# Kernel tuning notes

Measured on AMD Instinct MI355X. Metric: run time of the kernel, lower is better.

The kernel has to match this reference:

```python
import jax, jax.numpy as jnp
import numpy as np

B, N, D = 32, 32768, 128

def setup_inputs() -> dict:
    key = jax.random.key(0)
    k1, k2, k3 = jax.random.split(key, 3)
    inputs = jax.random.normal(k1, (B, D), dtype=jnp.float32)
    # alphas must be in (0,1): variance = 1 - alpha
    alphas = jax.random.uniform(k2, (B,), dtype=jnp.float32, minval=0.05, maxval=0.95)
    data_batch = jax.random.normal(k3, (N, D), dtype=jnp.float32)
    return {"inputs": inputs, "alphas": alphas, "data_batch": data_batch}

def reference(inputs, alphas, data_batch):
    # inputs: [B, D], alphas: [B], data_batch: [N, D]
    d = inputs.shape[-1]
    sqrt_a = jnp.sqrt(alphas)[:, None]          # [B, 1]
    var = (1.0 - alphas)[:, None]                # [B, 1]
    # means = sqrt(alpha) * data -> [B, N, D]; squared distance summed over D
    diff = inputs[:, None, :] - sqrt_a[:, :, None] * data_batch[None]  # [B, N, D]
    sq = jnp.sum(diff * diff, axis=-1)           # [B, N]
    # logits summed over feature dim: -(0.5*D*log(var) + 0.5/var * sq)
    logits = -(0.5 * d * jnp.log(var) + 0.5 / var * sq)  # [B, N]
    probs = jax.nn.softmax(logits, axis=1)       # [B, N]
    x0 = probs @ data_batch                      # [B, D]
    return (inputs - sqrt_a * x0) / jnp.sqrt(var)
```

## Files before the change

kernel.cpp:

```cpp
#include <hip/hip_runtime.h>
#include <math.h>

#define BB 32
#define DD 128
#define NN 32768

#define NB1 1024
#define T1 256
#define ROWS 32
#define WS_STRIDE 132
#define NP NB1

__global__ __launch_bounds__(T1) void bayes_k1(
    const float* __restrict__ inputs, const float* __restrict__ alphas,
    const float* __restrict__ data, float* __restrict__ ws)
{
    __shared__ float4 tile[ROWS * 32];
    __shared__ float  ms[2][16][2];

    const int tid  = threadIdx.x;
    const int lane = tid & 63;
    const int wv   = tid >> 6;
    const int half = wv >> 1;
    const int wr   = wv & 1;
    const int br   = lane >> 2;
    const int q    = lane & 3;
    const int b    = half * 16 + br;
    const int bid  = blockIdx.x;

    const float alpha = alphas[b];
    const float sa    = sqrtf(alpha);
    const float var   = 1.0f - alpha;
    const float c1    = sa / var;
    const float c2    = 0.5f * alpha / var;

    const float4* g4 = (const float4*)data + (size_t)bid * (ROWS * DD / 4);
    {
        float4 v[4];
        #pragma unroll
        for (int k = 0; k < 4; ++k) v[k] = g4[k * T1 + tid];
        #pragma unroll
        for (int k = 0; k < 4; ++k) {
            const int f = k * T1 + tid;
            const int r = f >> 5, c = f & 31;
            tile[r * 32 + (c ^ ((r & 7) << 2))] = v[k];
        }
    }

    float4 in4[8];
    {
        const float4* ig = (const float4*)inputs + b * 32;
        #pragma unroll
        for (int j = 0; j < 8; ++j) in4[j] = ig[4 * j + q];
    }

    __syncthreads();

    float nn = 0.0f;
    {
        const int r = wr * 16 + (lane >> 2);
        const int sw = (r & 7) << 2;
        #pragma unroll
        for (int j = 0; j < 8; ++j) {
            const float4 d = tile[r * 32 + ((4 * j + q) ^ sw)];
            nn = fmaf(d.x, d.x, nn); nn = fmaf(d.y, d.y, nn);
            nn = fmaf(d.z, d.z, nn); nn = fmaf(d.w, d.w, nn);
        }
        nn += __shfl_xor(nn, 1);
        nn += __shfl_xor(nn, 2);
    }

    float m = -INFINITY, s = 0.0f;
    float4 acc[8];
    #pragma unroll
    for (int j = 0; j < 8; ++j) acc[j] = make_float4(0.f, 0.f, 0.f, 0.f);

    #pragma unroll 4
    for (int rl = 0; rl < 16; ++rl) {
        const int r  = wr * 16 + rl;
        const int sw = (r & 7) << 2;

        float4 d4[8];
        #pragma unroll
        for (int j = 0; j < 8; ++j) d4[j] = tile[r * 32 + ((4 * j + q) ^ sw)];

        float4 dv = make_float4(0.f, 0.f, 0.f, 0.f);
        #pragma unroll
        for (int j = 0; j < 8; ++j) {
            dv.x = fmaf(in4[j].x, d4[j].x, dv.x);
            dv.y = fmaf(in4[j].y, d4[j].y, dv.y);
            dv.z = fmaf(in4[j].z, d4[j].z, dv.z);
            dv.w = fmaf(in4[j].w, d4[j].w, dv.w);
        }
        float dot = (dv.x + dv.y) + (dv.z + dv.w);
        dot += __shfl_xor(dot, 1);
        dot += __shfl_xor(dot, 2);

        const float nr    = __shfl(nn, rl << 2);
        const float logit = c1 * dot - c2 * nr;

        float pp = logit - m;
        if (pp > 10.0f) {
            const float sc = __expf(-pp);
            s *= sc;
            #pragma unroll
            for (int j = 0; j < 8; ++j) {
                acc[j].x *= sc; acc[j].y *= sc; acc[j].z *= sc; acc[j].w *= sc;
            }
            m = logit; pp = 0.0f;
        }
        const float wgt = __expf(pp);
        s += wgt;
        #pragma unroll
        for (int j = 0; j < 8; ++j) {
            acc[j].x = fmaf(wgt, d4[j].x, acc[j].x);
            acc[j].y = fmaf(wgt, d4[j].y, acc[j].y);
            acc[j].z = fmaf(wgt, d4[j].z, acc[j].z);
            acc[j].w = fmaf(wgt, d4[j].w, acc[j].w);
        }
    }

    __syncthreads();
    float* red = (float*)tile;
    if (wr == 1) {
        if (q == 0) { ms[half][br][0] = m; ms[half][br][1] = s; }
        float4* rp = (float4*)(red + half * 2048 + br * 128);
        const int sw = (br & 7) << 2;
        #pragma unroll
        for (int j = 0; j < 8; ++j) rp[(4 * j + q) ^ sw] = acc[j];
    }
    __syncthreads();
    if (wr == 0) {
        const float mo = ms[half][br][0], so = ms[half][br][1];
        const float M  = fmaxf(m, mo);
        const float e0 = __expf(m - M), e1 = __expf(mo - M);
        s = s * e0 + so * e1;
        const float4* rp = (const float4*)(red + half * 2048 + br * 128);
        const int sw = (br & 7) << 2;
        #pragma unroll
        for (int j = 0; j < 8; ++j) {
            const float4 d = rp[(4 * j + q) ^ sw];
            acc[j].x = acc[j].x * e0 + e1 * d.x;
            acc[j].y = acc[j].y * e0 + e1 * d.y;
            acc[j].z = acc[j].z * e0 + e1 * d.z;
            acc[j].w = acc[j].w * e0 + e1 * d.w;
        }
        m = M;

        float* wsp = ws + ((size_t)bid * BB + b) * WS_STRIDE;
        if (q == 0) { wsp[0] = m; wsp[1] = s; }
        float4* wa = (float4*)(wsp + 4);
        #pragma unroll
        for (int j = 0; j < 8; ++j) wa[4 * j + q] = acc[j];
    }
}

__global__ __launch_bounds__(256) void bayes_k2(
    const float* __restrict__ inputs, const float* __restrict__ alphas,
    const float* __restrict__ ws, float* __restrict__ out)
{
    const int b   = blockIdx.x >> 2;
    const int dq  = blockIdx.x & 3;
    const int tid = threadIdx.x;

    __shared__ float e_s[NP];
    __shared__ float red_s[16];
    __shared__ float part[8][32];

    float mi[4], si[4];
    #pragma unroll
    for (int k = 0; k < 4; ++k) {
        const int i = tid + k * 256;
        const size_t idx = ((size_t)i * BB + b) * WS_STRIDE;
        mi[k] = ws[idx];
        si[k] = ws[idx + 1];
    }

    float mm = fmaxf(fmaxf(mi[0], mi[1]), fmaxf(mi[2], mi[3]));
    #pragma unroll
    for (int off = 1; off <= 32; off <<= 1) mm = fmaxf(mm, __shfl_xor(mm, off));
    if ((tid & 63) == 0) red_s[tid >> 6] = mm;
    __syncthreads();
    const float M = fmaxf(fmaxf(red_s[0], red_s[1]), fmaxf(red_s[2], red_s[3]));

    float ss = 0.0f;
    #pragma unroll
    for (int k = 0; k < 4; ++k) {
        const float ei = __expf(mi[k] - M);
        e_s[tid + k * 256] = ei;
        ss = fmaf(si[k], ei, ss);
    }
    #pragma unroll
    for (int off = 1; off <= 32; off <<= 1) ss += __shfl_xor(ss, off);
    if ((tid & 63) == 0) red_s[8 + (tid >> 6)] = ss;
    __syncthreads();
    const float S = (red_s[8] + red_s[9]) + (red_s[10] + red_s[11]);

    const int dd = tid & 31, ii = tid >> 5;
    const int d  = dq * 32 + dd;
    float x = 0.0f;
    #pragma unroll 8
    for (int k = 0; k < 128; ++k) {
        const int i = ii + k * 8;
        x = fmaf(e_s[i], ws[((size_t)i * BB + b) * WS_STRIDE + 4 + d], x);
    }
    part[ii][dd] = x;
    __syncthreads();

    if (tid < 32) {
        float x0 = 0.0f;
        #pragma unroll
        for (int p = 0; p < 8; ++p) x0 += part[p][tid];
        x0 /= S;
        const float alpha = alphas[b];
        const float sa  = sqrtf(alpha);
        const float var = 1.0f - alpha;
        const int dout  = dq * 32 + tid;
        out[b * DD + dout] = (inputs[b * DD + dout] - sa * x0) / sqrtf(var);
    }
}

extern "C" void kernel_launch(void* const* d_in, const int* in_sizes, int n_in,
                              void* d_out, int out_size, void* d_ws, size_t ws_size,
                              hipStream_t stream)
{
    const float* inputs = (const float*)d_in[0];
    const float* alphas = (const float*)d_in[1];
    const float* data   = (const float*)d_in[2];
    float* out = (float*)d_out;
    float* ws  = (float*)d_ws;

    bayes_k1<<<NB1, T1, 0, stream>>>(inputs, alphas, data, ws);
    bayes_k2<<<BB * 4, 256, 0, stream>>>(inputs, alphas, ws, out);
}
```

Baseline: 97.17 us.

## Compute logits and weighted sums with bf16 MFMA using split-precision operands

Rewrites the partial-softmax kernel so the data-input dot products run on MFMA 16x16x32 bf16 instructions. Both data and inputs are split into hi and lo bf16 parts to keep close to fp32 accuracy, and the probability-weighted sum runs as a second MFMA using bf16 exps and transposed data. Each block now covers 64 rows with one-shot softmax instead of 32 rows with online rescaling, which halves the partial count that the combine kernel reads, and the workspace layout becomes batch-major. The cost is bf16 rounding in the second GEMM, a strided transposed global load, and a much larger LDS footprint that can lower occupancy.

```diff
diff --git a/kernel.cpp b/kernel.cpp
--- a/kernel.cpp
+++ b/kernel.cpp
@@ -5,153 +5,249 @@
 #define DD 128
 #define NN 32768
 
-#define NB1 1024
-#define T1 256
-#define ROWS 32
-#define WS_STRIDE 132
-#define NP NB1
-
-__global__ __launch_bounds__(T1) void bayes_k1(
+#define NB 512
+#define RPB 64
+#define WS_STRIDE 136
+#define NP NB
+
+typedef __attribute__((ext_vector_type(8))) short bf16x8;
+typedef __attribute__((ext_vector_type(4))) float f32x4;
+
+#define O_RH   0
+#define O_RL   16384
+#define O_INH  32768
+#define O_INL  40960
+#define O_RT   49152
+#define O_D1   65536
+#define O_NRM  75776
+#define O_PT   O_INH
+#define O_X0   O_RH
+#define ARENA  76032
+
+__device__ __forceinline__ unsigned bf16_rne(float x) {
+    unsigned u = __builtin_bit_cast(unsigned, x);
+    return (u + 0x7FFFu + ((u >> 16) & 1u)) >> 16;
+}
+__device__ __forceinline__ float bf16f(unsigned h) {
+    return __builtin_bit_cast(float, h << 16);
+}
+__device__ __forceinline__ unsigned pk2(float a, float b) {
+    return bf16_rne(a) | (bf16_rne(b) << 16);
+}
+
+__global__ __launch_bounds__(256) void bayes_k1(
     const float* __restrict__ inputs, const float* __restrict__ alphas,
     const float* __restrict__ data, float* __restrict__ ws)
 {
-    __shared__ float4 tile[ROWS * 32];
-    __shared__ float  ms[2][16][2];
+    __shared__ __align__(16) char arena[ARENA];
 
     const int tid  = threadIdx.x;
     const int lane = tid & 63;
     const int wv   = tid >> 6;
-    const int half = wv >> 1;
-    const int wr   = wv & 1;
-    const int br   = lane >> 2;
-    const int q    = lane & 3;
-    const int b    = half * 16 + br;
+    const int ln   = lane & 15;
+    const int g    = lane >> 4;
     const int bid  = blockIdx.x;
 
-    const float alpha = alphas[b];
-    const float sa    = sqrtf(alpha);
-    const float var   = 1.0f - alpha;
-    const float c1    = sa / var;
-    const float c2    = 0.5f * alpha / var;
-
-    const float4* g4 = (const float4*)data + (size_t)bid * (ROWS * DD / 4);
-    {
-        float4 v[4];
-        #pragma unroll
-        for (int k = 0; k < 4; ++k) v[k] = g4[k * T1 + tid];
-        #pragma unroll
-        for (int k = 0; k < 4; ++k) {
-            const int f = k * T1 + tid;
-            const int r = f >> 5, c = f & 31;
-            tile[r * 32 + (c ^ ((r & 7) << 2))] = v[k];
-        }
-    }
-
-    float4 in4[8];
-    {
-        const float4* ig = (const float4*)inputs + b * 32;
-        #pragma unroll
-        for (int j = 0; j < 8; ++j) in4[j] = ig[4 * j + q];
-    }
-
-    __syncthreads();
-
-    float nn = 0.0f;
-    {
-        const int r = wr * 16 + (lane >> 2);
-        const int sw = (r & 7) << 2;
-        #pragma unroll
-        for (int j = 0; j < 8; ++j) {
-            const float4 d = tile[r * 32 + ((4 * j + q) ^ sw)];
-            nn = fmaf(d.x, d.x, nn); nn = fmaf(d.y, d.y, nn);
-            nn = fmaf(d.z, d.z, nn); nn = fmaf(d.w, d.w, nn);
-        }
+    {
+        const int r = tid >> 2, c4 = tid & 3;
+        const float4* gp = (const float4*)(data + ((size_t)bid * RPB + r) * DD + c4 * 32);
+        float v[32];
+        #pragma unroll
+        for (int i = 0; i < 8; ++i) {
+            const float4 t4 = gp[i];
+            v[4*i+0] = t4.x; v[4*i+1] = t4.y; v[4*i+2] = t4.z; v[4*i+3] = t4.w;
+        }
+        float nn = 0.0f;
+        #pragma unroll
+        for (int i = 0; i < 32; ++i) nn = fmaf(v[i], v[i], nn);
         nn += __shfl_xor(nn, 1);
         nn += __shfl_xor(nn, 2);
-    }
-
-    float m = -INFINITY, s = 0.0f;
-    float4 acc[8];
-    #pragma unroll
-    for (int j = 0; j < 8; ++j) acc[j] = make_float4(0.f, 0.f, 0.f, 0.f);
-
-    #pragma unroll 4
-    for (int rl = 0; rl < 16; ++rl) {
-        const int r  = wr * 16 + rl;
-        const int sw = (r & 7) << 2;
-
-        float4 d4[8];
-        #pragma unroll
-        for (int j = 0; j < 8; ++j) d4[j] = tile[r * 32 + ((4 * j + q) ^ sw)];
-
-        float4 dv = make_float4(0.f, 0.f, 0.f, 0.f);
-        #pragma unroll
-        for (int j = 0; j < 8; ++j) {
-            dv.x = fmaf(in4[j].x, d4[j].x, dv.x);
-            dv.y = fmaf(in4[j].y, d4[j].y, dv.y);
-            dv.z = fmaf(in4[j].z, d4[j].z, dv.z);
-            dv.w = fmaf(in4[j].w, d4[j].w, dv.w);
-        }
-        float dot = (dv.x + dv.y) + (dv.z + dv.w);
-        dot += __shfl_xor(dot, 1);
-        dot += __shfl_xor(dot, 2);
-
-        const float nr    = __shfl(nn, rl << 2);
-        const float logit = c1 * dot - c2 * nr;
-
-        float pp = logit - m;
-        if (pp > 10.0f) {
-            const float sc = __expf(-pp);
-            s *= sc;
-            #pragma unroll
-            for (int j = 0; j < 8; ++j) {
-                acc[j].x *= sc; acc[j].y *= sc; acc[j].z *= sc; acc[j].w *= sc;
-            }
-            m = logit; pp = 0.0f;
-        }
-        const float wgt = __expf(pp);
-        s += wgt;
-        #pragma unroll
-        for (int j = 0; j < 8; ++j) {
-            acc[j].x = fmaf(wgt, d4[j].x, acc[j].x);
-            acc[j].y = fmaf(wgt, d4[j].y, acc[j].y);
-            acc[j].z = fmaf(wgt, d4[j].z, acc[j].z);
-            acc[j].w = fmaf(wgt, d4[j].w, acc[j].w);
-        }
-    }
-
-    __syncthreads();
-    float* red = (float*)tile;
-    if (wr == 1) {
-        if (q == 0) { ms[half][br][0] = m; ms[half][br][1] = s; }
-        float4* rp = (float4*)(red + half * 2048 + br * 128);
-        const int sw = (br & 7) << 2;
-        #pragma unroll
-        for (int j = 0; j < 8; ++j) rp[(4 * j + q) ^ sw] = acc[j];
-    }
-    __syncthreads();
-    if (wr == 0) {
-        const float mo = ms[half][br][0], so = ms[half][br][1];
-        const float M  = fmaxf(m, mo);
-        const float e0 = __expf(m - M), e1 = __expf(mo - M);
-        s = s * e0 + so * e1;
-        const float4* rp = (const float4*)(red + half * 2048 + br * 128);
-        const int sw = (br & 7) << 2;
-        #pragma unroll
-        for (int j = 0; j < 8; ++j) {
-            const float4 d = rp[(4 * j + q) ^ sw];
-            acc[j].x = acc[j].x * e0 + e1 * d.x;
-            acc[j].y = acc[j].y * e0 + e1 * d.y;
-            acc[j].z = acc[j].z * e0 + e1 * d.z;
-            acc[j].w = acc[j].w * e0 + e1 * d.w;
-        }
-        m = M;
-
-        float* wsp = ws + ((size_t)bid * BB + b) * WS_STRIDE;
-        if (q == 0) { wsp[0] = m; wsp[1] = s; }
-        float4* wa = (float4*)(wsp + 4);
-        #pragma unroll
-        for (int j = 0; j < 8; ++j) wa[4 * j + q] = acc[j];
+        if (c4 == 0) *(float*)(arena + O_NRM + r * 4) = nn;
+
+        const int swz = (r & 7) << 4;
+        #pragma unroll
+        for (int u = 0; u < 4; ++u) {
+            unsigned hw[4], lw[4];
+            #pragma unroll
+            for (int j = 0; j < 4; ++j) {
+                const float a = v[u*8 + 2*j], b = v[u*8 + 2*j + 1];
+                const unsigned ah = bf16_rne(a), bh = bf16_rne(b);
+                hw[j] = ah | (bh << 16);
+                lw[j] = pk2(a - bf16f(ah), b - bf16f(bh));
+            }
+            const int go = (c4 * 64 + u * 16) ^ swz;
+            *(uint4*)(arena + O_RH + r * 256 + go) = make_uint4(hw[0], hw[1], hw[2], hw[3]);
+            *(uint4*)(arena + O_RL + r * 256 + go) = make_uint4(lw[0], lw[1], lw[2], lw[3]);
+        }
+    }
+
+    {
+        const int b = tid >> 3, c8 = tid & 7;
+        const float4* gp = (const float4*)(inputs + b * DD + c8 * 16);
+        float v[16];
+        #pragma unroll
+        for (int i = 0; i < 4; ++i) {
+            const float4 t4 = gp[i];
+            v[4*i+0] = t4.x; v[4*i+1] = t4.y; v[4*i+2] = t4.z; v[4*i+3] = t4.w;
+        }
+        const int swz = (b & 7) << 4;
+        #pragma unroll
+        for (int u = 0; u < 2; ++u) {
+            unsigned hw[4], lw[4];
+            #pragma unroll
+            for (int j = 0; j < 4; ++j) {
+                const float a = v[u*8 + 2*j], bb = v[u*8 + 2*j + 1];
+                const unsigned ah = bf16_rne(a), bh = bf16_rne(bb);
+                hw[j] = ah | (bh << 16);
+                lw[j] = pk2(a - bf16f(ah), bb - bf16f(bh));
+            }
+            const int go = (c8 * 32 + u * 16) ^ swz;
+            *(uint4*)(arena + O_INH + b * 256 + go) = make_uint4(hw[0], hw[1], hw[2], hw[3]);
+            *(uint4*)(arena + O_INL + b * 256 + go) = make_uint4(lw[0], lw[1], lw[2], lw[3]);
+        }
+    }
+
+    {
+        const int d = tid >> 1, rh = tid & 1;
+        const float* gc = data + ((size_t)bid * RPB + rh * 32) * DD + d;
+        const int swz = (d & 7) << 4;
+        #pragma unroll
+        for (int u = 0; u < 4; ++u) {
+            unsigned w[4];
+            #pragma unroll
+            for (int j = 0; j < 4; ++j)
+                w[j] = pk2(gc[(u*8 + 2*j) * DD], gc[(u*8 + 2*j + 1) * DD]);
+            *(uint4*)(arena + O_RT + d * 128 + ((rh * 64 + u * 16) ^ swz)) =
+                make_uint4(w[0], w[1], w[2], w[3]);
+        }
+    }
+    __syncthreads();
+
+    const int ni = wv & 1;
+    const int kh = wv >> 1;
+    f32x4 acc1[4];
+    #pragma unroll
+    for (int mt = 0; mt < 4; ++mt)
+        #pragma unroll
+        for (int i = 0; i < 4; ++i) acc1[mt][i] = 0.0f;
+
+    #pragma unroll
+    for (int ks = 0; ks < 2; ++ks) {
+        const int kbyte = kh * 128 + ks * 64 + g * 16;
+        const int n = ni * 16 + ln;
+        const bf16x8 Bh = *(const bf16x8*)(arena + O_INH + n * 256 + (kbyte ^ ((n & 7) << 4)));
+        const bf16x8 Bl = *(const bf16x8*)(arena + O_INL + n * 256 + (kbyte ^ ((n & 7) << 4)));
+        #pragma unroll
+        for (int mt = 0; mt < 4; ++mt) {
+            const int r = mt * 16 + ln;
+            const bf16x8 Ah = *(const bf16x8*)(arena + O_RH + r * 256 + (kbyte ^ ((r & 7) << 4)));
+            const bf16x8 Al = *(const bf16x8*)(arena + O_RL + r * 256 + (kbyte ^ ((r & 7) << 4)));
+            acc1[mt] = __builtin_amdgcn_mfma_f32_16x16x32_bf16(Ah, Bh, acc1[mt], 0, 0, 0);
+            acc1[mt] = __builtin_amdgcn_mfma_f32_16x16x32_bf16(Al, Bh, acc1[mt], 0, 0, 0);
+            acc1[mt] = __builtin_amdgcn_mfma_f32_16x16x32_bf16(Ah, Bl, acc1[mt], 0, 0, 0);
+        }
+    }
+    if (kh == 1) {
+        #pragma unroll
+        for (int mt = 0; mt < 4; ++mt)
+            *(f32x4*)(arena + O_D1 + ((ni * 4 + mt) * 16 + ln) * 80 + g * 16) = acc1[mt];
+    }
+    __syncthreads();
+
+    if (kh == 0) {
+        const int b = ni * 16 + ln;
+        #pragma unroll
+        for (int mt = 0; mt < 4; ++mt) {
+            const f32x4 o = *(const f32x4*)(arena + O_D1 + ((ni * 4 + mt) * 16 + ln) * 80 + g * 16);
+            #pragma unroll
+            for (int i = 0; i < 4; ++i) acc1[mt][i] += o[i];
+        }
+        const float alpha = alphas[b];
+        const float var = 1.0f - alpha;
+        const float c1 = sqrtf(alpha) / var;
+        const float c2 = 0.5f * alpha / var;
+
+        float lg[4][4];
+        float mx = -1e30f;
+        #pragma unroll
+        for (int mt = 0; mt < 4; ++mt) {
+            const f32x4 nr4 = *(const f32x4*)(arena + O_NRM + (mt * 16 + g * 4) * 4);
+            #pragma unroll
+            for (int i = 0; i < 4; ++i) {
+                lg[mt][i] = fmaf(c1, acc1[mt][i], -c2 * nr4[i]);
+                mx = fmaxf(mx, lg[mt][i]);
+            }
+        }
+        mx = fmaxf(mx, __shfl_xor(mx, 16));
+        mx = fmaxf(mx, __shfl_xor(mx, 32));
+
+        float ss = 0.0f;
+        const int swz = (b & 7) << 4;
+        #pragma unroll
+        for (int mt = 0; mt < 4; ++mt) {
+            float e0 = __expf(lg[mt][0] - mx), e1 = __expf(lg[mt][1] - mx);
+            float e2 = __expf(lg[mt][2] - mx), e3 = __expf(lg[mt][3] - mx);
+            ss += (e0 + e1) + (e2 + e3);
+            *(uint2*)(arena + O_PT + b * 128 + ((mt * 32 + g * 8) ^ swz)) =
+                make_uint2(pk2(e0, e1), pk2(e2, e3));
+        }
+        ss += __shfl_xor(ss, 16);
+        ss += __shfl_xor(ss, 32);
+        if (g == 0) {
+            float* wsp = ws + ((size_t)b * NB + bid) * WS_STRIDE;
+            wsp[0] = mx; wsp[1] = ss;
+        }
+    }
+    __syncthreads();
+
+    {
+        f32x4 acc2[2][2];
+        #pragma unroll
+        for (int a = 0; a < 2; ++a)
+            #pragma unroll
+            for (int c = 0; c < 2; ++c)
+                #pragma unroll
+                for (int i = 0; i < 4; ++i) acc2[a][c][i] = 0.0f;
+
+        #pragma unroll
+        for (int ks = 0; ks < 2; ++ks) {
+            bf16x8 Bp[2];
+            #pragma unroll
+            for (int nt = 0; nt < 2; ++nt) {
+                const int b2 = nt * 16 + ln;
+                Bp[nt] = *(const bf16x8*)(arena + O_PT + b2 * 128 +
+                                          ((ks * 64 + g * 16) ^ ((b2 & 7) << 4)));
+            }
+            #pragma unroll
+            for (int mt2 = 0; mt2 < 2; ++mt2) {
+                const int d = wv * 32 + mt2 * 16 + ln;
+                const bf16x8 Ar = *(const bf16x8*)(arena + O_RT + d * 128 +
+                                                   ((ks * 64 + g * 16) ^ ((d & 7) << 4)));
+                #pragma unroll
+                for (int nt = 0; nt < 2; ++nt)
+                    acc2[mt2][nt] = __builtin_amdgcn_mfma_f32_16x16x32_bf16(Ar, Bp[nt], acc2[mt2][nt], 0, 0, 0);
+            }
+        }
+        #pragma unroll
+        for (int mt2 = 0; mt2 < 2; ++mt2)
+            #pragma unroll
+            for (int nt = 0; nt < 2; ++nt) {
+                const int b = nt * 16 + ln;
+                const int d0 = wv * 32 + mt2 * 16 + g * 4;
+                *(f32x4*)(arena + O_X0 + b * 512 + ((d0 * 4) ^ ((b & 7) << 4))) = acc2[mt2][nt];
+            }
+    }
+    __syncthreads();
+
+    {
+        const int b = tid >> 3, c8 = tid & 7;
+        const int swz = (b & 7) << 4;
+        float* dst = ws + ((size_t)b * NB + bid) * WS_STRIDE + 4 + c8 * 16;
+        #pragma unroll
+        for (int u = 0; u < 4; ++u) {
+            const f32x4 v = *(const f32x4*)(arena + O_X0 + b * 512 + ((c8 * 64 + u * 16) ^ swz));
+            *(f32x4*)(dst + u * 4) = v;
+        }
     }
 }
 
@@ -167,16 +263,17 @@
     __shared__ float red_s[16];
     __shared__ float part[8][32];
 
-    float mi[4], si[4];
-    #pragma unroll
-    for (int k = 0; k < 4; ++k) {
-        const int i = tid + k * 256;
-        const size_t idx = ((size_t)i * BB + b) * WS_STRIDE;
-        mi[k] = ws[idx];
-        si[k] = ws[idx + 1];
-    }
-
-    float mm = fmaxf(fmaxf(mi[0], mi[1]), fmaxf(mi[2], mi[3]));
+    const float* base_b = ws + (size_t)b * NP * WS_STRIDE;
+
+    float mi[2], si[2];
+    #pragma unroll
+    for (int q = 0; q < 2; ++q) {
+        const int i = tid + q * 256;
+        mi[q] = base_b[(size_t)i * WS_STRIDE];
+        si[q] = base_b[(size_t)i * WS_STRIDE + 1];
+    }
+
+    float mm = fmaxf(mi[0], mi[1]);
     #pragma unroll
     for (int off = 1; off <= 32; off <<= 1) mm = fmaxf(mm, __shfl_xor(mm, off));
     if ((tid & 63) == 0) red_s[tid >> 6] = mm;
@@ -185,10 +282,10 @@
 
     float ss = 0.0f;
     #pragma unroll
-    for (int k = 0; k < 4; ++k) {
-        const float ei = __expf(mi[k] - M);
-        e_s[tid + k * 256] = ei;
-        ss = fmaf(si[k], ei, ss);
+    for (int q = 0; q < 2; ++q) {
+        const float ei = __expf(mi[q] - M);
+        e_s[tid + q * 256] = ei;
+        ss = fmaf(si[q], ei, ss);
     }
     #pragma unroll
     for (int off = 1; off <= 32; off <<= 1) ss += __shfl_xor(ss, off);
@@ -200,9 +297,9 @@
     const int d  = dq * 32 + dd;
     float x = 0.0f;
     #pragma unroll 8
-    for (int k = 0; k < 128; ++k) {
+    for (int k = 0; k < 64; ++k) {
         const int i = ii + k * 8;
-        x = fmaf(e_s[i], ws[((size_t)i * BB + b) * WS_STRIDE + 4 + d], x);
+        x = fmaf(e_s[i], base_b[(size_t)i * WS_STRIDE + 4 + d], x);
     }
     part[ii][dd] = x;
     __syncthreads();
@@ -230,6 +327,6 @@
     float* out = (float*)d_out;
     float* ws  = (float*)d_ws;
 
-    bayes_k1<<<NB1, T1, 0, stream>>>(inputs, alphas, data, ws);
+    bayes_k1<<<NB, 256, 0, stream>>>(inputs, alphas, data, ws);
     bayes_k2<<<BB * 4, 256, 0, stream>>>(inputs, alphas, ws, out);
 }
```

Result: faster. 83.28 us (-14.3%).
